# Kernel tuning notes

Measured on AMD Instinct MI355X. Metric: run time of the kernel, lower is better.

Reference implementation:

```python
import jax, jax.numpy as jnp
import numpy as np

TOP_K = 8
N_EXPERTS = 64
ALPHA = 0.001
EPS = 1e-9


def setup_inputs() -> dict:
    key = jax.random.key(0)
    k1, k2 = jax.random.split(key)
    B, S, H, E = 4, 4096, 2048, N_EXPERTS
    hidden_states = jax.random.normal(k1, (B, S, H), dtype=jnp.float32)
    # kaiming_uniform_(a=sqrt(5)) on [E,H] -> bound = 1/sqrt(H)
    bound = 1.0 / np.sqrt(H)
    weight = jax.random.uniform(k2, (E, H), dtype=jnp.float32, minval=-bound, maxval=bound)
    return {"hidden_states": hidden_states, "weight": weight}


def reference(hidden_states, weight):
    B, S, H = hidden_states.shape
    E = weight.shape[0]
    x = hidden_states.reshape(-1, H)                     # [N, H], N = B*S
    logits = jnp.einsum('nh,eh->ne', x, weight)          # [N, E]
    scores = jax.nn.sigmoid(logits)                      # sigmoid affinity (DeepSeek-V3 style)

    topk_weight, topk_idx = jax.lax.top_k(scores, TOP_K)  # [N, K]
    # norm_topk_prob = True and top_k > 1
    denom = topk_weight.sum(axis=-1, keepdims=True) + EPS
    topk_weight = topk_weight / denom

    # aux load-balance loss (training, alpha > 0); scatter-count instead of one_hot
    N = x.shape[0]
    counts = jnp.zeros((E,), dtype=jnp.float32).at[topk_idx.reshape(-1)].add(1.0)
    load = counts / (N * TOP_K)                          # == one_hot.mean(dim=(0,1))
    prob_raw = scores / (scores.sum(axis=-1, keepdims=True) + EPS)
    prob = prob_raw.mean(axis=0)
    prob = prob / (prob.sum() + EPS)
    aux_loss = ALPHA * (load * prob).sum() * E

    return topk_idx, topk_weight, aux_loss
```

## Files before the change

kernel.cpp:

```cpp
#include <hip/hip_runtime.h>
#include <math.h>

#define N_TOK 16384
#define HDIM  2048
#define NEXP  64
#define TOPK  8
#define NKS   4
#define KSEG  (HDIM / NKS)
#define KCH   32
#define NCH   (KSEG / KCH)

#define PART_OFF  0
#define STATS_OFF (33u << 20)

typedef double d4 __attribute__((ext_vector_type(4)));

__device__ __forceinline__ int derive_flag() {
    const int l = threadIdx.x & 63;
    const int i16 = l & 15, q = l >> 4;
    const int r4 = l >> 2,  m4 = l & 3;
    int fv = 0;
#pragma unroll
    for (int ai = 0; ai < 2; ++ai)
#pragma unroll
    for (int bi = 0; bi < 2; ++bi) {
        const int ra = ai ? r4 : i16, ka = ai ? m4 : q;
        const int cb = bi ? r4 : i16, kb = bi ? m4 : q;
        double a = (double)(ra * 4 + ka + 1);
        double b = (double)((kb + 1) * 100 + 3 * cb);
        d4 acc = {0., 0., 0., 0.};
        acc = __builtin_amdgcn_mfma_f64_16x16x4f64(a, b, acc, 0, 0, 0);
#pragma unroll
        for (int sf = 0; sf < 2; ++sf)
#pragma unroll
        for (int tr = 0; tr < 2; ++tr) {
            int ok = 1;
#pragma unroll
            for (int r = 0; r < 4; ++r) {
                const int p   = sf ? (q + 4 * r) : (4 * q + r);
                const int row = tr ? i16 : p;
                const int col = tr ? p : i16;
                double ref = 0.0;
#pragma unroll
                for (int k = 0; k < 4; ++k)
                    ref += (double)(row * 4 + k + 1) * (double)((k + 1) * 100 + 3 * col);
                ok &= (acc[r] == ref);
            }
            if (__all(ok) && fv == 0) fv = 1 + ai * 8 + bi * 4 + sf * 2 + tr;
        }
    }
    return fv;
}

__global__ __launch_bounds__(512, 8) void gemm_mfma_kernel(const float* __restrict__ X,
                                                           const float* __restrict__ W,
                                                           double* __restrict__ part) {
    const int f = derive_flag();
    if (f == 0) return;
    const int fb = f - 1;
    const int ai = (fb >> 3) & 1, bi = (fb >> 2) & 1;
    const int sf = (fb >> 1) & 1, tr = fb & 1;

    const int tt  = blockIdx.x >> 2;
    const int ks  = blockIdx.x & 3;
    const int tid = threadIdx.x;
    const int l   = tid & 63;
    const int wv  = tid >> 6;
    const int wr  = wv >> 2;
    const int wc  = wv & 3;
    const int tok0 = tt * 64;
    const int k0   = ks * KSEG;

    const int i16 = l & 15, q = l >> 4, r4 = l >> 2, m4 = l & 3;
    const int ra = ai ? r4 : i16, ka = ai ? m4 : q;
    const int cb = bi ? r4 : i16, kb = bi ? m4 : q;

    __shared__ double Xs[64][34];
    __shared__ double Ws[64][34];

    d4 acc0 = {0., 0., 0., 0.};
    d4 acc1 = {0., 0., 0., 0.};

    const int sr = tid >> 3;
    const int sc = (tid & 7) * 4;
    const float* xg = X + (size_t)(tok0 + sr) * HDIM + k0 + sc;
    const float* wg = W + (size_t)sr * HDIM + k0 + sc;

    float4 px = *(const float4*)xg;
    float4 pw = *(const float4*)wg;

    for (int c = 0; c < NCH; ++c) {
        __syncthreads();
        {
            double2 d0, d1;
            d0.x = (double)px.x; d0.y = (double)px.y;
            d1.x = (double)px.z; d1.y = (double)px.w;
            *(double2*)&Xs[sr][sc]     = d0;
            *(double2*)&Xs[sr][sc + 2] = d1;
            d0.x = (double)pw.x; d0.y = (double)pw.y;
            d1.x = (double)pw.z; d1.y = (double)pw.w;
            *(double2*)&Ws[sr][sc]     = d0;
            *(double2*)&Ws[sr][sc + 2] = d1;
        }
        __syncthreads();
        if (c + 1 < NCH) {
            px = *(const float4*)(xg + (c + 1) * KCH);
            pw = *(const float4*)(wg + (c + 1) * KCH);
        }
        const double* pa0 = &Xs[wr * 32 + ra][ka];
        const double* pa1 = &Xs[wr * 32 + 16 + ra][ka];
        const double* pb0 = &Ws[wc * 16 + cb][kb];
#pragma unroll
        for (int kq = 0; kq < 8; ++kq) {
            double a0 = pa0[4 * kq];
            double a1 = pa1[4 * kq];
            double b0 = pb0[4 * kq];
            acc0 = __builtin_amdgcn_mfma_f64_16x16x4f64(a0, b0, acc0, 0, 0, 0);
            acc1 = __builtin_amdgcn_mfma_f64_16x16x4f64(a1, b0, acc1, 0, 0, 0);
        }
    }

    double* pbase = part + (size_t)ks * N_TOK * NEXP;
#pragma unroll
    for (int rt = 0; rt < 2; ++rt) {
        const d4 accv = rt == 0 ? acc0 : acc1;
#pragma unroll
        for (int r = 0; r < 4; ++r) {
            const int p    = sf ? (q + 4 * r) : (4 * q + r);
            const int dtok = tr ? i16 : p;
            const int dex  = tr ? p : i16;
            const int tok  = tok0 + wr * 32 + rt * 16 + dtok;
            const int ex   = wc * 16 + dex;
            pbase[(size_t)tok * NEXP + ex] = accv[r];
        }
    }
}

__global__ __launch_bounds__(512, 4) void gemm_valu_kernel(const float* __restrict__ X,
                                                           const float* __restrict__ W,
                                                           double* __restrict__ part,
                                                           float* __restrict__ stats) {
    if (blockIdx.x == 0 && threadIdx.x < 128)
        stats[threadIdx.x] = 0.f;
    if (derive_flag() != 0) return;
    const int tt   = blockIdx.x >> 2;
    const int ks   = blockIdx.x & 3;
    const int tid  = threadIdx.x;
    const int lane = tid & 63;
    const int wv   = tid >> 6;
    const int tok0 = tt * 64;
    const int k0   = ks * KSEG;

    __shared__ double xs[64][18];
    __shared__ double wsh[16][66];

    double acc[8];
#pragma unroll
    for (int t = 0; t < 8; ++t) acc[t] = 0.0;

    const int sx_tok = tid >> 3;
    const int sx_k   = (tid & 7) * 2;
    const float* xg  = X + (size_t)(tok0 + sx_tok) * HDIM + k0 + sx_k;
    const int sw_k = tid >> 5;
    const int sw_e = (tid & 31) * 2;
    const float* wg0 = W + (size_t)sw_e * HDIM + k0 + sw_k;
    const float* wg1 = W + (size_t)(sw_e + 1) * HDIM + k0 + sw_k;

    float2 px = *(const float2*)xg;
    float  pa = *wg0, pb2 = *wg1;

    for (int c = 0; c < KSEG / 16; ++c) {
        __syncthreads();
        {
            double2 xv; xv.x = (double)px.x; xv.y = (double)px.y;
            *(double2*)&xs[sx_tok][sx_k] = xv;
            double2 wv2; wv2.x = (double)pa; wv2.y = (double)pb2;
            *(double2*)&wsh[sw_k][sw_e] = wv2;
        }
        __syncthreads();
        if (c + 1 < KSEG / 16) {
            px  = *(const float2*)(xg + (c + 1) * 16);
            pa  = wg0[(c + 1) * 16];
            pb2 = wg1[(c + 1) * 16];
        }
        double wr_[16];
#pragma unroll
        for (int j = 0; j < 16; ++j) wr_[j] = wsh[j][lane];
#pragma unroll
        for (int t = 0; t < 8; ++t) {
            const int trr = wv * 8 + t;
#pragma unroll
            for (int kp = 0; kp < 8; ++kp) {
                double2 xv = *(const double2*)&xs[trr][kp * 2];
                acc[t] = fma(xv.x, wr_[kp * 2],     acc[t]);
                acc[t] = fma(xv.y, wr_[kp * 2 + 1], acc[t]);
            }
        }
    }

    double* pb = part + ((size_t)ks * N_TOK + tok0 + wv * 8) * NEXP + lane;
#pragma unroll
    for (int t = 0; t < 8; ++t)
        pb[(size_t)t * NEXP] = acc[t];
}

__global__ __launch_bounds__(256) void topk_kernel(const double* __restrict__ part,
                                                   float* __restrict__ outIdx,
                                                   float* __restrict__ outW,
                                                   float* __restrict__ stats) {
    __shared__ float sc_s[16][65];
    __shared__ float lds_counts[NEXP];
    __shared__ float psum_part[4][NEXP];
    const int tid  = threadIdx.x;
    const int lane = tid & 63;
    const int w    = tid >> 6;
    if (tid < NEXP) lds_counts[tid] = 0.f;

    const int t0 = blockIdx.x * 16;
#pragma unroll
    for (int p = 0; p < 4; ++p) {
        const int idx = p * 256 + tid;
        const int t   = idx >> 6;
        const int e   = idx & 63;
        const double* pp = part + ((size_t)(t0 + t)) * NEXP + e;
        double l = (pp[0] + pp[(size_t)N_TOK * NEXP]) +
                   (pp[2 * (size_t)N_TOK * NEXP] + pp[3 * (size_t)N_TOK * NEXP]);
        sc_s[t][e] = (float)(1.0 / (1.0 + exp(-l)));
    }
    __syncthreads();

    float ps = 0.f;
#pragma unroll
    for (int i = 0; i < 4; i += 2) {
        const int tA = w * 4 + i, tB = tA + 1;
        float sA = sc_s[tA][lane], sB = sc_s[tB][lane];

        float rsA = sA, rsB = sB;
#pragma unroll
        for (int off = 32; off; off >>= 1) {
            rsA += __shfl_xor(rsA, off);
            rsB += __shfl_xor(rsB, off);
        }
        ps += sA / (rsA + 1e-9f) + sB / (rsB + 1e-9f);

        float curA = sA, curB = sB;
        float denA = 0.f, denB = 0.f;
        int   wiA = 0, wiB = 0;
        float wvA = 0.f, wvB = 0.f;
#pragma unroll
        for (int k = 0; k < TOPK; ++k) {
            float mA = curA; int miA = lane;
            float mB = curB; int miB = lane;
#pragma unroll
            for (int off = 32; off; off >>= 1) {
                float omA = __shfl_xor(mA, off);
                int   oiA = __shfl_xor(miA, off);
                float omB = __shfl_xor(mB, off);
                int   oiB = __shfl_xor(miB, off);
                if (omA > mA || (omA == mA && oiA < miA)) { mA = omA; miA = oiA; }
                if (omB > mB || (omB == mB && oiB < miB)) { mB = omB; miB = oiB; }
            }
            denA += mA; denB += mB;
            if (lane == k)   { wiA = miA; wvA = mA; wiB = miB; wvB = mB; }
            if (lane == miA) curA = -1e30f;
            if (lane == miB) curB = -1e30f;
        }
        if (lane < TOPK) {
            const int ta = t0 + tA, tb = t0 + tB;
            outIdx[(size_t)ta * TOPK + lane] = (float)wiA;
            outW  [(size_t)ta * TOPK + lane] = wvA / (denA + 1e-9f);
            outIdx[(size_t)tb * TOPK + lane] = (float)wiB;
            outW  [(size_t)tb * TOPK + lane] = wvB / (denB + 1e-9f);
            atomicAdd(&lds_counts[wiA], 1.f);
            atomicAdd(&lds_counts[wiB], 1.f);
        }
    }
    psum_part[w][lane] = ps;
    __syncthreads();
    if (tid < NEXP) {
        float tot = psum_part[0][tid] + psum_part[1][tid] +
                    psum_part[2][tid] + psum_part[3][tid];
        atomicAdd(&stats[tid], tot);
        atomicAdd(&stats[NEXP + tid], lds_counts[tid]);
    }
}

__global__ void aux_kernel(const float* __restrict__ stats, float* __restrict__ out) {
    const int e = threadIdx.x;
    float prob = stats[e] / (float)N_TOK;
    float cnt  = stats[NEXP + e];
    float loadf = cnt / ((float)N_TOK * TOPK);
    float S = prob;
#pragma unroll
    for (int off = 32; off; off >>= 1) S += __shfl_xor(S, off);
    float pn = prob / (S + 1e-9f);
    float v  = loadf * pn;
#pragma unroll
    for (int off = 32; off; off >>= 1) v += __shfl_xor(v, off);
    if (e == 0) out[2 * N_TOK * TOPK] = 0.001f * v * (float)NEXP;
}

extern "C" void kernel_launch(void* const* d_in, const int* in_sizes, int n_in,
                              void* d_out, int out_size, void* d_ws, size_t ws_size,
                              hipStream_t stream) {
    (void)in_sizes; (void)n_in; (void)out_size; (void)ws_size;
    const float* X = (const float*)d_in[0];
    const float* W = (const float*)d_in[1];
    float* out = (float*)d_out;
    char*  ws  = (char*)d_ws;
    double* part  = (double*)(ws + PART_OFF);
    float*  stats = (float*)(ws + STATS_OFF);

    gemm_mfma_kernel<<<1024, 512, 0, stream>>>(X, W, part);
    gemm_valu_kernel<<<1024, 512, 0, stream>>>(X, W, part, stats);
    topk_kernel<<<1024, 256, 0, stream>>>(part, out, out + N_TOK * TOPK, stats);
    aux_kernel<<<1, 64, 0, stream>>>(stats, out);
}
```

Measured before the change: 133.8 us.

## Double-buffer LDS tiles in f64 MFMA gating GEMM with two-ahead prefetch

Shared-memory staging tiles become ping-pong buffers, and global loads are prefetched into registers two chunks ahead. This drops the loop to one barrier per chunk and lets the convert-and-store of the next tile overlap the MFMA work on the current one. LDS per block roughly doubles, and launch bounds drop from 8 to 4 blocks per multiprocessor hint. Resident blocks per CU may fall, which could offset the latency hiding gained.

New measurement: 131.7 us (median of 2 runs). No clear change (-1.5%).

```diff
diff --git a/kernel.cpp b/kernel.cpp
--- a/kernel.cpp
+++ b/kernel.cpp
@@ -52,7 +52,36 @@
     return fv;
 }
 
-__global__ __launch_bounds__(512, 8) void gemm_mfma_kernel(const float* __restrict__ X,
+__device__ __forceinline__ void stage_store(double (*Xb)[34], double (*Wb)[34],
+                                            int sr, int sc, float4 px, float4 pw) {
+    double2 d0, d1;
+    d0.x = (double)px.x; d0.y = (double)px.y;
+    d1.x = (double)px.z; d1.y = (double)px.w;
+    *(double2*)&Xb[sr][sc]     = d0;
+    *(double2*)&Xb[sr][sc + 2] = d1;
+    d0.x = (double)pw.x; d0.y = (double)pw.y;
+    d1.x = (double)pw.z; d1.y = (double)pw.w;
+    *(double2*)&Wb[sr][sc]     = d0;
+    *(double2*)&Wb[sr][sc + 2] = d1;
+}
+
+__device__ __forceinline__ void mfma_chunk(const double (*Xb)[34], const double (*Wb)[34],
+                                           int wr, int wc, int ra, int cb, int ka, int kb,
+                                           d4& acc0, d4& acc1) {
+    const double* qa0 = &Xb[wr * 32 + ra][ka];
+    const double* qa1 = &Xb[wr * 32 + 16 + ra][ka];
+    const double* qb0 = &Wb[wc * 16 + cb][kb];
+#pragma unroll
+    for (int kq = 0; kq < 8; ++kq) {
+        double a0 = qa0[4 * kq];
+        double a1 = qa1[4 * kq];
+        double b0 = qb0[4 * kq];
+        acc0 = __builtin_amdgcn_mfma_f64_16x16x4f64(a0, b0, acc0, 0, 0, 0);
+        acc1 = __builtin_amdgcn_mfma_f64_16x16x4f64(a1, b0, acc1, 0, 0, 0);
+    }
+}
+
+__global__ __launch_bounds__(512, 4) void gemm_mfma_kernel(const float* __restrict__ X,
                                                            const float* __restrict__ W,
                                                            double* __restrict__ part) {
     const int f = derive_flag();
@@ -75,8 +104,8 @@
     const int ra = ai ? r4 : i16, ka = ai ? m4 : q;
     const int cb = bi ? r4 : i16, kb = bi ? m4 : q;
 
-    __shared__ double Xs[64][34];
-    __shared__ double Ws[64][34];
+    __shared__ double Xs[2][64][34];
+    __shared__ double Ws[2][64][34];
 
     d4 acc0 = {0., 0., 0., 0.};
     d4 acc1 = {0., 0., 0., 0.};
@@ -86,37 +115,29 @@
     const float* xg = X + (size_t)(tok0 + sr) * HDIM + k0 + sc;
     const float* wg = W + (size_t)sr * HDIM + k0 + sc;
 
-    float4 px = *(const float4*)xg;
-    float4 pw = *(const float4*)wg;
-
-    for (int c = 0; c < NCH; ++c) {
+    float4 pxA = *(const float4*)xg;
+    float4 pwA = *(const float4*)wg;
+    float4 pxB = *(const float4*)(xg + KCH);
+    float4 pwB = *(const float4*)(wg + KCH);
+    stage_store(Xs[0], Ws[0], sr, sc, pxA, pwA);
+    __syncthreads();
+
+    for (int c = 0; c < NCH; c += 2) {
+        if (c + 2 < NCH) {
+            pxA = *(const float4*)(xg + (c + 2) * KCH);
+            pwA = *(const float4*)(wg + (c + 2) * KCH);
+        }
+        mfma_chunk(Xs[0], Ws[0], wr, wc, ra, cb, ka, kb, acc0, acc1);
+        stage_store(Xs[1], Ws[1], sr, sc, pxB, pwB);
         __syncthreads();
-        {
-            double2 d0, d1;
-            d0.x = (double)px.x; d0.y = (double)px.y;
-            d1.x = (double)px.z; d1.y = (double)px.w;
-            *(double2*)&Xs[sr][sc]     = d0;
-            *(double2*)&Xs[sr][sc + 2] = d1;
-            d0.x = (double)pw.x; d0.y = (double)pw.y;
-            d1.x = (double)pw.z; d1.y = (double)pw.w;
-            *(double2*)&Ws[sr][sc]     = d0;
-            *(double2*)&Ws[sr][sc + 2] = d1;
-        }
-        __syncthreads();
-        if (c + 1 < NCH) {
-            px = *(const float4*)(xg + (c + 1) * KCH);
-            pw = *(const float4*)(wg + (c + 1) * KCH);
-        }
-        const double* pa0 = &Xs[wr * 32 + ra][ka];
-        const double* pa1 = &Xs[wr * 32 + 16 + ra][ka];
-        const double* pb0 = &Ws[wc * 16 + cb][kb];
-#pragma unroll
-        for (int kq = 0; kq < 8; ++kq) {
-            double a0 = pa0[4 * kq];
-            double a1 = pa1[4 * kq];
-            double b0 = pb0[4 * kq];
-            acc0 = __builtin_amdgcn_mfma_f64_16x16x4f64(a0, b0, acc0, 0, 0, 0);
-            acc1 = __builtin_amdgcn_mfma_f64_16x16x4f64(a1, b0, acc1, 0, 0, 0);
+        if (c + 3 < NCH) {
+            pxB = *(const float4*)(xg + (c + 3) * KCH);
+            pwB = *(const float4*)(wg + (c + 3) * KCH);
+        }
+        mfma_chunk(Xs[1], Ws[1], wr, wc, ra, cb, ka, kb, acc0, acc1);
+        if (c + 2 < NCH) {
+            stage_store(Xs[0], Ws[0], sr, sc, pxA, pwA);
+            __syncthreads();
         }
     }
 
```
